# Optimization experiments

Hardware: AMD Instinct MI355X
Metric: run time of the kernel (lower is better)

## Reference

```python
import jax, jax.numpy as jnp
import numpy as np

N_LAYERS = 2
D_MODEL = 1024
D_INNER = 2048  # expand=2
D_STATE = 16
D_CONV = 4
DT_RANK = 64    # ceil(d_model/16)
N_CLASSES = 10
B, L = 4, 1024


def setup_inputs() -> dict:
    key = jax.random.key(0)
    ks = jax.random.split(key, 20)
    s = 0.02
    inp = {
        'x': jax.random.normal(ks[0], (B, L, D_MODEL), jnp.float32),
        'ln1_w': jnp.ones((N_LAYERS, D_MODEL), jnp.float32),
        'ln1_b': jnp.zeros((N_LAYERS, D_MODEL), jnp.float32),
        'in_proj_w': jax.random.normal(ks[1], (N_LAYERS, 2 * D_INNER, D_MODEL), jnp.float32) * s,
        'conv_w': jax.random.normal(ks[2], (N_LAYERS, D_INNER, D_CONV), jnp.float32) * 0.2,
        'conv_b': jnp.zeros((N_LAYERS, D_INNER), jnp.float32),
        'x_proj_w': jax.random.normal(ks[3], (N_LAYERS, DT_RANK + 2 * D_STATE, D_INNER), jnp.float32) * s,
        'dt_proj_w': jax.random.normal(ks[4], (N_LAYERS, D_INNER, DT_RANK), jnp.float32) * 0.1,
        'dt_proj_b': jax.random.normal(ks[5], (N_LAYERS, D_INNER), jnp.float32) * 0.1 - 4.6,  # softplus -> dt ~ 0.01
        'A_log': jnp.broadcast_to(jnp.log(jnp.arange(1, D_STATE + 1, dtype=jnp.float32)), (N_LAYERS, D_INNER, D_STATE)) + 0.0,
        'D_param': jnp.ones((N_LAYERS, D_INNER), jnp.float32),
        'out_proj_w': jax.random.normal(ks[6], (N_LAYERS, D_MODEL, D_INNER), jnp.float32) * s,
        'norm_w': jnp.ones((D_MODEL,), jnp.float32),
        'norm_b': jnp.zeros((D_MODEL,), jnp.float32),
        'head_w': jax.random.normal(ks[7], (N_CLASSES, D_MODEL), jnp.float32) * s,
        'head_b': jnp.zeros((N_CLASSES,), jnp.float32),
    }
    return inp


def _layernorm(x, w, b, eps=1e-5):
    mu = jnp.mean(x, axis=-1, keepdims=True)
    var = jnp.var(x, axis=-1, keepdims=True)
    return (x - mu) * jax.lax.rsqrt(var + eps) * w + b


def _selective_scan(xc, dt, A, Bm, Cm, D):
    # xc, dt: (B, L, D_INNER); Bm, Cm: (B, L, D_STATE); A: (D_INNER, D_STATE); D: (D_INNER,)
    def step(h, inp):
        dt_t, B_t, C_t, xc_t = inp  # (B,C),(B,N),(B,N),(B,C)
        dA = jnp.exp(dt_t[..., None] * A)            # (B, C, N)
        h = dA * h + (dt_t * xc_t)[..., None] * B_t[:, None, :]
        y = jnp.einsum('bcn,bn->bc', h, C_t)
        return h, y

    h0 = jnp.zeros((xc.shape[0], A.shape[0], A.shape[1]), xc.dtype)
    xs = (dt.transpose(1, 0, 2), Bm.transpose(1, 0, 2), Cm.transpose(1, 0, 2), xc.transpose(1, 0, 2))
    _, ys = jax.lax.scan(step, h0, xs)
    y = ys.transpose(1, 0, 2)  # (B, L, C)
    return y + xc * D


def _mamba_layer(x, ln_w, ln_b, in_w, cw, cb, xp_w, dtp_w, dtp_b, A_log, D, out_w):
    h = _layernorm(x, ln_w, ln_b)
    xz = jnp.einsum('bld,ed->ble', h, in_w)          # (B, L, 2*D_INNER)
    x_in, z = jnp.split(xz, 2, axis=-1)
    # causal depthwise conv1d, kernel D_CONV
    xp = jnp.pad(x_in, ((0, 0), (D_CONV - 1, 0), (0, 0)))
    conv = cb
    for k in range(D_CONV):
        conv = conv + cw[:, k] * xp[:, k:k + x_in.shape[1], :]
    xc = jax.nn.silu(conv)
    x_dbl = jnp.einsum('blc,ec->ble', xc, xp_w)
    dt_r = x_dbl[..., :DT_RANK]
    Bm = x_dbl[..., DT_RANK:DT_RANK + D_STATE]
    Cm = x_dbl[..., DT_RANK + D_STATE:]
    dt = jax.nn.softplus(jnp.einsum('blr,cr->blc', dt_r, dtp_w) + dtp_b)
    A = -jnp.exp(A_log)
    y = _selective_scan(xc, dt, A, Bm, Cm, D)
    y = y * jax.nn.silu(z)
    return x + jnp.einsum('blc,dc->bld', y, out_w)


def reference(x, ln1_w, ln1_b, in_proj_w, conv_w, conv_b, x_proj_w, dt_proj_w, dt_proj_b,
              A_log, D_param, out_proj_w, norm_w, norm_b, head_w, head_b):
    for i in range(N_LAYERS):
        x = _mamba_layer(x, ln1_w[i], ln1_b[i], in_proj_w[i], conv_w[i], conv_b[i],
                         x_proj_w[i], dt_proj_w[i], dt_proj_b[i], A_log[i], D_param[i], out_proj_w[i])
    x = _layernorm(x, norm_w, norm_b)
    pooled = jnp.mean(x, axis=1)  # (B, D_MODEL)
    return pooled @ head_w.T + head_b
```

## Files before the change

kernel.cpp:

```cpp
#include <hip/hip_runtime.h>
#include <hip/hip_bf16.h>

#define N_LAYERS 2
#define D_MODEL 1024
#define D_INNER 2048
#define D_STATE 16
#define D_CONV 4
#define DT_RANK 64
#define N_CLASSES 10
#define BB 4
#define LL 1024
#define BL (BB*LL)
#define CH 32
#define CLEN (LL/CH)
#define KS 8
#define KSO 2

typedef __attribute__((ext_vector_type(8))) short bf16x8;
typedef __attribute__((ext_vector_type(8))) unsigned short us8;
typedef __attribute__((ext_vector_type(4))) float f32x4;

typedef const void __attribute__((address_space(1)))* gas_ptr;
typedef void __attribute__((address_space(3)))* las_ptr;
#define GLDS16(g, p) __builtin_amdgcn_global_load_lds((gas_ptr)(g), (las_ptr)(p), 16, 0, 0)

__device__ inline unsigned short rnd_bf16(float x) {
  unsigned u = __float_as_uint(x);
  return (unsigned short)((u + 0x7FFFu + ((u >> 16) & 1u)) >> 16);
}
__device__ inline float b2f(unsigned short u) {
  return __uint_as_float(((unsigned)u) << 16);
}

__global__ __launch_bounds__(256) void round_k(const float* __restrict__ in,
    unsigned short* __restrict__ hi) {
  const int i = blockIdx.x * 256 + threadIdx.x;
  const float4 v = ((const float4*)in)[i];
  ushort4 h4;
  h4.x = rnd_bf16(v.x); h4.y = rnd_bf16(v.y);
  h4.z = rnd_bf16(v.z); h4.w = rnd_bf16(v.w);
  ((ushort4*)hi)[i] = h4;
}

__global__ __launch_bounds__(256) void layernorm_bf16_k(const float* __restrict__ x,
    const float* __restrict__ w, const float* __restrict__ b,
    unsigned short* __restrict__ oh) {
  const int row = blockIdx.x;
  const int t = threadIdx.x;
  const float4 v = *(const float4*)(x + (size_t)row * D_MODEL + t * 4);
  float s = v.x + v.y + v.z + v.w;
  float q = v.x*v.x + v.y*v.y + v.z*v.z + v.w*v.w;
  #pragma unroll
  for (int o = 32; o; o >>= 1) { s += __shfl_down(s, o); q += __shfl_down(q, o); }
  __shared__ float red[8];
  if ((t & 63) == 0) { red[t >> 6] = s; red[4 + (t >> 6)] = q; }
  __syncthreads();
  s = red[0] + red[1] + red[2] + red[3];
  q = red[4] + red[5] + red[6] + red[7];
  const float mean = s * (1.f / D_MODEL);
  const float var  = q * (1.f / D_MODEL) - mean * mean;
  const float rstd = rsqrtf(var + 1e-5f);
  const float4 wv = *(const float4*)(w + t * 4);
  const float4 bv = *(const float4*)(b + t * 4);
  ushort4 h4;
  h4.x = rnd_bf16((v.x - mean) * rstd * wv.x + bv.x);
  h4.y = rnd_bf16((v.y - mean) * rstd * wv.y + bv.y);
  h4.z = rnd_bf16((v.z - mean) * rstd * wv.z + bv.z);
  h4.w = rnd_bf16((v.w - mean) * rstd * wv.w + bv.w);
  ((ushort4*)(oh + (size_t)row * D_MODEL))[t] = h4;
}

template<int OUT>
__global__ __launch_bounds__(256) void oreduce_ln_k(
    const float* __restrict__ part, const float* __restrict__ Xin,
    float* __restrict__ Xout,
    const float* __restrict__ w, const float* __restrict__ b,
    void* __restrict__ out) {
  const int row = blockIdx.x;
  const int t = threadIdx.x;
  float4 v = *(const float4*)(Xin + (size_t)row * D_MODEL + t * 4);
  #pragma unroll
  for (int k = 0; k < KSO; k++) {
    const float4 p = *(const float4*)(part + (size_t)k * BL * D_MODEL
                                      + (size_t)row * D_MODEL + t * 4);
    v.x += p.x; v.y += p.y; v.z += p.z; v.w += p.w;
  }
  *(float4*)(Xout + (size_t)row * D_MODEL + t * 4) = v;
  float s = v.x + v.y + v.z + v.w;
  float q = v.x*v.x + v.y*v.y + v.z*v.z + v.w*v.w;
  #pragma unroll
  for (int o = 32; o; o >>= 1) { s += __shfl_down(s, o); q += __shfl_down(q, o); }
  __shared__ float red[8];
  if ((t & 63) == 0) { red[t >> 6] = s; red[4 + (t >> 6)] = q; }
  __syncthreads();
  s = red[0] + red[1] + red[2] + red[3];
  q = red[4] + red[5] + red[6] + red[7];
  const float mean = s * (1.f / D_MODEL);
  const float var  = q * (1.f / D_MODEL) - mean * mean;
  const float rstd = rsqrtf(var + 1e-5f);
  const float4 wv = *(const float4*)(w + t * 4);
  const float4 bv = *(const float4*)(b + t * 4);
  float4 o4;
  o4.x = (v.x - mean) * rstd * wv.x + bv.x;
  o4.y = (v.y - mean) * rstd * wv.y + bv.y;
  o4.z = (v.z - mean) * rstd * wv.z + bv.z;
  o4.w = (v.w - mean) * rstd * wv.w + bv.w;
  if constexpr (OUT == 0) {
    ushort4 h4;
    h4.x = rnd_bf16(o4.x); h4.y = rnd_bf16(o4.y);
    h4.z = rnd_bf16(o4.z); h4.w = rnd_bf16(o4.w);
    ((ushort4*)((unsigned short*)out + (size_t)row * D_MODEL))[t] = h4;
  } else {
    *(float4*)((float*)out + (size_t)row * D_MODEL + t * 4) = o4;
  }
}

template<int EPI, int KSEG>
__global__ __launch_bounds__(256) void mfma_gemm_nt(
    const unsigned short* __restrict__ Ah, const unsigned short* __restrict__ Bh,
    void* __restrict__ Cv, int M, int N, int K, int ldc) {
  __shared__ unsigned short As[128 * 64];
  __shared__ unsigned short Bs[128 * 64];
  const int tid = threadIdx.x;
  const int w = tid >> 6, l = tid & 63;
  const int wr = w >> 1, wc = w & 1;
  const int nbx = gridDim.x;
  const int nwg = nbx * gridDim.y;
  int bid = blockIdx.y * nbx + blockIdx.x;
  bid = (bid & 7) * (nwg >> 3) + (bid >> 3);
  const int st = bid >> 6, wi = bid & 63;
  const int stpr = nbx >> 3;
  const int n0 = ((st % stpr) * 8 + (wi & 7)) * 128;
  const int m0 = ((st / stpr) * 8 + (wi >> 3)) * 128;
  const int kz = (KSEG > 1) ? blockIdx.z : 0;
  const int kbeg = kz * (K / KSEG);
  const int kend = kbeg + K / KSEG;
  const int srow = l >> 3;
  const int scol = (l & 7) * 8;
  const int fr = l & 15;
  const int fk = (l >> 4) * 8;
  f32x4 acc[4][4] = {};

  #pragma unroll 1
  for (int k0 = kbeg; k0 < kend; k0 += 64) {
    __syncthreads();
    #pragma unroll
    for (int it = 0; it < 4; ++it) {
      const int bi = it * 4 + w;
      const int row = bi * 8 + srow;
      GLDS16(Ah + (size_t)(m0 + row) * K + k0 + scol, &As[bi * 512 + l * 8]);
      GLDS16(Bh + (size_t)(n0 + row) * K + k0 + scol, &Bs[bi * 512 + l * 8]);
    }
    __syncthreads();
    #pragma unroll
    for (int kk = 0; kk < 64; kk += 32) {
      bf16x8 a[4], b[4];
      #pragma unroll
      for (int f = 0; f < 4; ++f)
        b[f] = *(const bf16x8*)&Bs[(wc * 64 + f * 16 + fr) * 64 + kk + fk];
      #pragma unroll
      for (int f = 0; f < 4; ++f)
        a[f] = *(const bf16x8*)&As[(wr * 64 + f * 16 + fr) * 64 + kk + fk];
      #pragma unroll
      for (int i = 0; i < 4; ++i)
        #pragma unroll
        for (int j = 0; j < 4; ++j)
          acc[i][j] = __builtin_amdgcn_mfma_f32_16x16x32_bf16(
              a[i], b[j], acc[i][j], 0, 0, 0);
    }
  }
  const int orow = (l >> 4) * 4;
  const int ocol = l & 15;
  if constexpr (EPI == 0) {
    unsigned short* Cw = (unsigned short*)Cv;
    #pragma unroll
    for (int i = 0; i < 4; ++i)
      #pragma unroll
      for (int j = 0; j < 4; ++j)
        #pragma unroll
        for (int r = 0; r < 4; ++r) {
          const int m = m0 + wr * 64 + i * 16 + orow + r;
          const int n = n0 + wc * 64 + j * 16 + ocol;
          Cw[(size_t)m * ldc + n] = rnd_bf16(acc[i][j][r]);
        }
  } else {
    float* Cw = (float*)Cv + (size_t)kz * M * ldc;
    #pragma unroll
    for (int i = 0; i < 4; ++i)
      #pragma unroll
      for (int j = 0; j < 4; ++j)
        #pragma unroll
        for (int r = 0; r < 4; ++r) {
          const int m = m0 + wr * 64 + i * 16 + orow + r;
          const int n = n0 + wc * 64 + j * 16 + ocol;
          Cw[(size_t)m * ldc + n] = acc[i][j][r];
        }
  }
}

template<int BM, int BN, int BK, int TM, int TN, int EPI>
__global__ __launch_bounds__(256) void sgemm_nt(
    const float* __restrict__ A, const float* __restrict__ B,
    void* __restrict__ Cv, int M, int N, int K, int lda, int ldb, int ldc,
    const float* __restrict__ bias) {
  constexpr int THREADS = 256;
  constexpr int NT = BN / TN;
  constexpr int K4 = BK / 4;
  constexpr int A_F4 = BM * BK / (THREADS * 4);
  constexpr int B_F4 = BN * BK / (THREADS * 4);
  static_assert((BM / TM) * (BN / TN) == THREADS, "thread shape");
  __shared__ float As[BK][BM + 4];
  __shared__ float Bs[BK][BN + 4];
  const int tid = threadIdx.x;
  const int m0 = blockIdx.y * BM;
  const int n0 = blockIdx.x * BN;
  const int tn = (tid % NT) * TN;
  const int tm = (tid / NT) * TM;
  float acc[TM][TN] = {};
  for (int k0 = 0; k0 < K; k0 += BK) {
    #pragma unroll
    for (int i = 0; i < A_F4; i++) {
      int li = tid + i * THREADS;
      int r = li / K4, c4 = li % K4;
      float4 v = *(const float4*)(A + (size_t)(m0 + r) * lda + k0 + c4 * 4);
      As[c4*4+0][r] = v.x; As[c4*4+1][r] = v.y; As[c4*4+2][r] = v.z; As[c4*4+3][r] = v.w;
    }
    #pragma unroll
    for (int i = 0; i < B_F4; i++) {
      int li = tid + i * THREADS;
      int r = li / K4, c4 = li % K4;
      float4 v = *(const float4*)(B + (size_t)(n0 + r) * ldb + k0 + c4 * 4);
      Bs[c4*4+0][r] = v.x; Bs[c4*4+1][r] = v.y; Bs[c4*4+2][r] = v.z; Bs[c4*4+3][r] = v.w;
    }
    __syncthreads();
    #pragma unroll
    for (int k = 0; k < BK; k++) {
      float a[TM], bf[TN];
      #pragma unroll
      for (int i = 0; i < TM; i++) a[i] = As[k][tm + i];
      #pragma unroll
      for (int j = 0; j < TN; j++) bf[j] = Bs[k][tn + j];
      #pragma unroll
      for (int i = 0; i < TM; i++)
        #pragma unroll
        for (int j = 0; j < TN; j++)
          acc[i][j] = fmaf(a[i], bf[j], acc[i][j]);
    }
    __syncthreads();
  }
  #pragma unroll
  for (int i = 0; i < TM; i++) {
    const int m = m0 + tm + i;
    #pragma unroll
    for (int j = 0; j < TN; j++) {
      const int n = n0 + tn + j;
      float v = acc[i][j];
      if constexpr (EPI == 1) {
        v += bias[n];
        v = (v > 20.f) ? v : log1pf(__expf(v));
        ((unsigned short*)Cv)[(size_t)m * ldc + n] = rnd_bf16(v);
      } else {
        ((float*)Cv)[(size_t)m * ldc + n] = v;
      }
    }
  }
}

__global__ __launch_bounds__(256) void sgemm_splitk_k(
    const unsigned short* __restrict__ A, const float* __restrict__ B,
    float* __restrict__ part) {
  __shared__ float As[32][64 + 4];
  __shared__ float Bs[32][32 + 4];
  const int tid = threadIdx.x;
  const int n0 = blockIdx.x * 32;
  const int m0 = blockIdx.y * 64;
  const int kz = blockIdx.z;
  const int tn = (tid & 15) * 2;
  const int tm = (tid >> 4) * 4;
  float acc[4][2] = {};
  for (int kb = 0; kb < 256; kb += 32) {
    const int k0 = kz * 256 + kb;
    {
      int r = tid >> 2, c8 = (tid & 3) * 8;
      us8 u = *(const us8*)(A + (size_t)(m0 + r) * D_INNER + k0 + c8);
      #pragma unroll
      for (int j = 0; j < 8; j++) As[c8 + j][r] = b2f((unsigned short)u[j]);
    }
    {
      int r = tid >> 3, c4 = tid & 7;
      float4 v = *(const float4*)(B + (size_t)(n0 + r) * D_INNER + k0 + c4 * 4);
      Bs[c4*4+0][r] = v.x; Bs[c4*4+1][r] = v.y;
      Bs[c4*4+2][r] = v.z; Bs[c4*4+3][r] = v.w;
    }
    __syncthreads();
    #pragma unroll
    for (int k = 0; k < 32; k++) {
      float a[4], bf[2];
      #pragma unroll
      for (int i = 0; i < 4; i++) a[i] = As[k][tm + i];
      bf[0] = Bs[k][tn]; bf[1] = Bs[k][tn + 1];
      #pragma unroll
      for (int i = 0; i < 4; i++) {
        acc[i][0] = fmaf(a[i], bf[0], acc[i][0]);
        acc[i][1] = fmaf(a[i], bf[1], acc[i][1]);
      }
    }
    __syncthreads();
  }
  float* p = part + (size_t)kz * BL * 96;
  #pragma unroll
  for (int i = 0; i < 4; i++) {
    const int m = m0 + tm + i;
    p[(size_t)m * 96 + n0 + tn]     = acc[i][0];
    p[(size_t)m * 96 + n0 + tn + 1] = acc[i][1];
  }
}

__global__ __launch_bounds__(256) void xproj_reduce_k(
    const float* __restrict__ part, float* __restrict__ out) {
  const int i = blockIdx.x * 256 + threadIdx.x;
  float s = 0.f;
  #pragma unroll
  for (int k = 0; k < KS; k++) s += part[(size_t)k * BL * 96 + i];
  out[i] = s;
}

__global__ __launch_bounds__(256) void conv_silu_k(
    const unsigned short* __restrict__ xz,
    const float* __restrict__ cw, const float* __restrict__ cb,
    unsigned short* __restrict__ xc) {
  const int gid = blockIdx.x * 256 + threadIdx.x;
  const int c4 = (gid & (D_INNER / 4 - 1)) << 2;
  const int row = gid >> 9;
  const int l = row & (LL - 1);
  const unsigned short* base = xz + (size_t)row * (2 * D_INNER) + c4;
  const float4 w0 = *(const float4*)(cw + (c4 + 0) * 4);
  const float4 w1 = *(const float4*)(cw + (c4 + 1) * 4);
  const float4 w2 = *(const float4*)(cw + (c4 + 2) * 4);
  const float4 w3 = *(const float4*)(cw + (c4 + 3) * 4);
  float4 acc = *(const float4*)(cb + c4);
  ushort4 uv = *(const ushort4*)base;
  acc.x = fmaf(w0.w, b2f(uv.x), acc.x); acc.y = fmaf(w1.w, b2f(uv.y), acc.y);
  acc.z = fmaf(w2.w, b2f(uv.z), acc.z); acc.w = fmaf(w3.w, b2f(uv.w), acc.w);
  if (l >= 1) {
    uv = *(const ushort4*)(base - 2 * D_INNER);
    acc.x = fmaf(w0.z, b2f(uv.x), acc.x); acc.y = fmaf(w1.z, b2f(uv.y), acc.y);
    acc.z = fmaf(w2.z, b2f(uv.z), acc.z); acc.w = fmaf(w3.z, b2f(uv.w), acc.w);
  }
  if (l >= 2) {
    uv = *(const ushort4*)(base - 4 * D_INNER);
    acc.x = fmaf(w0.y, b2f(uv.x), acc.x); acc.y = fmaf(w1.y, b2f(uv.y), acc.y);
    acc.z = fmaf(w2.y, b2f(uv.z), acc.z); acc.w = fmaf(w3.y, b2f(uv.w), acc.w);
  }
  if (l >= 3) {
    uv = *(const ushort4*)(base - 6 * D_INNER);
    acc.x = fmaf(w0.x, b2f(uv.x), acc.x); acc.y = fmaf(w1.x, b2f(uv.y), acc.y);
    acc.z = fmaf(w2.x, b2f(uv.z), acc.z); acc.w = fmaf(w3.x, b2f(uv.w), acc.w);
  }
  ushort4 o4;
  o4.x = rnd_bf16(acc.x / (1.f + __expf(-acc.x)));
  o4.y = rnd_bf16(acc.y / (1.f + __expf(-acc.y)));
  o4.z = rnd_bf16(acc.z / (1.f + __expf(-acc.z)));
  o4.w = rnd_bf16(acc.w / (1.f + __expf(-acc.w)));
  *(ushort4*)(xc + (size_t)row * D_INNER + c4) = o4;
}

__global__ __launch_bounds__(256) void scan_pass1_k(
    const unsigned short* __restrict__ dt, const unsigned short* __restrict__ xc,
    const float* __restrict__ xdbl, const float* __restrict__ A_log,
    float* __restrict__ hend, float* __restrict__ sumdt) {
  const int c = blockIdx.x * 256 + threadIdx.x;
  const int k = blockIdx.y;
  const int b = blockIdx.z;
  float Ac[D_STATE];
  #pragma unroll
  for (int n = 0; n < D_STATE; n++) Ac[n] = -__expf(A_log[c * D_STATE + n]);
  float h[D_STATE] = {};
  float sd = 0.f;
  const size_t r0 = (size_t)b * LL + (size_t)k * CLEN;
  const unsigned short* dtp = dt + r0 * D_INNER + c;
  const unsigned short* xcp = xc + r0 * D_INNER + c;
  const float* Bp  = xdbl + r0 * 96 + DT_RANK;

  float dtv = b2f(dtp[0]);
  float xv  = b2f(xcp[0]);
  float4 B0 = *(const float4*)(Bp + 0);
  float4 B1 = *(const float4*)(Bp + 4);
  float4 B2 = *(const float4*)(Bp + 8);
  float4 B3 = *(const float4*)(Bp + 12);
  for (int l = 0; l < CLEN; l++) {
    const int lp = (l + 1 < CLEN) ? l + 1 : l;
    const float dtv2 = b2f(dtp[(size_t)lp * D_INNER]);
    const float xv2  = b2f(xcp[(size_t)lp * D_INNER]);
    const float4 B0n = *(const float4*)(Bp + (size_t)lp * 96 + 0);
    const float4 B1n = *(const float4*)(Bp + (size_t)lp * 96 + 4);
    const float4 B2n = *(const float4*)(Bp + (size_t)lp * 96 + 8);
    const float4 B3n = *(const float4*)(Bp + (size_t)lp * 96 + 12);
    sd += dtv;
    const float dx = dtv * xv;
    const float Bv[D_STATE] = {B0.x,B0.y,B0.z,B0.w, B1.x,B1.y,B1.z,B1.w,
                               B2.x,B2.y,B2.z,B2.w, B3.x,B3.y,B3.z,B3.w};
    #pragma unroll
    for (int n = 0; n < D_STATE; n++)
      h[n] = fmaf(__expf(dtv * Ac[n]), h[n], dx * Bv[n]);
    dtv = dtv2; xv = xv2; B0 = B0n; B1 = B1n; B2 = B2n; B3 = B3n;
  }
  float* he = hend + (((size_t)(b * CH + k) * D_INNER + c) << 4);
  #pragma unroll
  for (int n = 0; n < D_STATE; n += 4)
    *(float4*)(he + n) = make_float4(h[n], h[n+1], h[n+2], h[n+3]);
  sumdt[(size_t)(b * CH + k) * D_INNER + c] = sd;
}

__global__ __launch_bounds__(256) void scan_fix_k(
    float* __restrict__ hend, const float* __restrict__ sumdt,
    const float* __restrict__ A_log) {
  const int gid = blockIdx.x * 256 + threadIdx.x;
  const int n = gid & 15;
  const int c = (gid >> 4) & (D_INNER - 1);
  const int b = gid >> 15;
  const float Ac = -__expf(A_log[c * D_STATE + n]);
  float hrun = 0.f;
  for (int k = 0; k < CH; k++) {
    const size_t base = (size_t)(b * CH + k) * D_INNER + c;
    const float sd = sumdt[base];
    float* hp = hend + (base << 4) + n;
    const float tmp = *hp;
    *hp = hrun;
    hrun = fmaf(__expf(Ac * sd), hrun, tmp);
  }
}

__global__ __launch_bounds__(256) void scan_pass3_k(
    const unsigned short* __restrict__ dt, const unsigned short* __restrict__ xc,
    const float* __restrict__ xdbl, const unsigned short* __restrict__ xz,
    const float* __restrict__ h0, const float* __restrict__ A_log,
    const float* __restrict__ Dp, unsigned short* __restrict__ yh) {
  const int c = blockIdx.x * 256 + threadIdx.x;
  const int k = blockIdx.y;
  const int b = blockIdx.z;
  float Ac[D_STATE];
  #pragma unroll
  for (int n = 0; n < D_STATE; n++) Ac[n] = -__expf(A_log[c * D_STATE + n]);
  const float Dv = Dp[c];
  float h[D_STATE];
  const float* hp = h0 + (((size_t)(b * CH + k) * D_INNER + c) << 4);
  #pragma unroll
  for (int n = 0; n < D_STATE; n += 4) {
    const float4 v = *(const float4*)(hp + n);
    h[n] = v.x; h[n+1] = v.y; h[n+2] = v.z; h[n+3] = v.w;
  }
  const size_t r0 = (size_t)b * LL + (size_t)k * CLEN;
  const unsigned short* dtp = dt + r0 * D_INNER + c;
  const unsigned short* xcp = xc + r0 * D_INNER + c;
  const float* Bp  = xdbl + r0 * 96 + DT_RANK;
  const unsigned short* zp = xz + r0 * (size_t)(2 * D_INNER) + D_INNER + c;
  unsigned short* yhp = yh + r0 * D_INNER + c;

  float dtv = b2f(dtp[0]);
  float xv  = b2f(xcp[0]);
  float zv  = b2f(zp[0]);
  float4 B0 = *(const float4*)(Bp + 0);
  float4 B1 = *(const float4*)(Bp + 4);
  float4 B2 = *(const float4*)(Bp + 8);
  float4 B3 = *(const float4*)(Bp + 12);
  float4 C0 = *(const float4*)(Bp + 16);
  float4 C1 = *(const float4*)(Bp + 20);
  float4 C2 = *(const float4*)(Bp + 24);
  float4 C3 = *(const float4*)(Bp + 28);
  for (int l = 0; l < CLEN; l++) {
    const int lp = (l + 1 < CLEN) ? l + 1 : l;
    const float dtv2 = b2f(dtp[(size_t)lp * D_INNER]);
    const float xv2  = b2f(xcp[(size_t)lp * D_INNER]);
    const float zv2  = b2f(zp[(size_t)lp * 2 * D_INNER]);
    const float4 B0n = *(const float4*)(Bp + (size_t)lp * 96 + 0);
    const float4 B1n = *(const float4*)(Bp + (size_t)lp * 96 + 4);
    const float4 B2n = *(const float4*)(Bp + (size_t)lp * 96 + 8);
    const float4 B3n = *(const float4*)(Bp + (size_t)lp * 96 + 12);
    const float4 C0n = *(const float4*)(Bp + (size_t)lp * 96 + 16);
    const float4 C1n = *(const float4*)(Bp + (size_t)lp * 96 + 20);
    const float4 C2n = *(const float4*)(Bp + (size_t)lp * 96 + 24);
    const float4 C3n = *(const float4*)(Bp + (size_t)lp * 96 + 28);
    const float dx = dtv * xv;
    const float Bv[D_STATE] = {B0.x,B0.y,B0.z,B0.w, B1.x,B1.y,B1.z,B1.w,
                               B2.x,B2.y,B2.z,B2.w, B3.x,B3.y,B3.z,B3.w};
    const float Cv[D_STATE] = {C0.x,C0.y,C0.z,C0.w, C1.x,C1.y,C1.z,C1.w,
                               C2.x,C2.y,C2.z,C2.w, C3.x,C3.y,C3.z,C3.w};
    float y = 0.f;
    #pragma unroll
    for (int n = 0; n < D_STATE; n++) {
      h[n] = fmaf(__expf(dtv * Ac[n]), h[n], dx * Bv[n]);
      y = fmaf(h[n], Cv[n], y);
    }
    y = fmaf(xv, Dv, y);
    y *= zv / (1.f + __expf(-zv));
    yhp[(size_t)l * D_INNER] = rnd_bf16(y);
    dtv = dtv2; xv = xv2; zv = zv2;
    B0 = B0n; B1 = B1n; B2 = B2n; B3 = B3n;
    C0 = C0n; C1 = C1n; C2 = C2n; C3 = C3n;
  }
}

__global__ __launch_bounds__(256) void pool1_k(const float* __restrict__ h,
    float* __restrict__ pp) {
  const int d = blockIdx.x * 256 + threadIdx.x;
  const int b = blockIdx.y;
  const int seg = blockIdx.z;
  float s = 0.f;
  const size_t base = (size_t)b * LL + (size_t)seg * 64;
  for (int l = 0; l < 64; l++) s += h[(base + l) * D_MODEL + d];
  pp[((size_t)(b * 16 + seg)) * D_MODEL + d] = s;
}
__global__ __launch_bounds__(256) void pool2_k(const float* __restrict__ pp,
    float* __restrict__ pooled) {
  const int d = blockIdx.x * 256 + threadIdx.x;
  const int b = blockIdx.y;
  float s = 0.f;
  #pragma unroll
  for (int k = 0; k < 16; k++) s += pp[((size_t)(b * 16 + k)) * D_MODEL + d];
  pooled[b * D_MODEL + d] = s * (1.f / LL);
}

__global__ __launch_bounds__(64) void head_k(const float* __restrict__ pooled,
    const float* __restrict__ hw, const float* __restrict__ hb,
    float* __restrict__ out) {
  const int b = blockIdx.x / N_CLASSES;
  const int j = blockIdx.x % N_CLASSES;
  float s = 0.f;
  for (int k = threadIdx.x; k < D_MODEL; k += 64)
    s = fmaf(pooled[b * D_MODEL + k], hw[j * D_MODEL + k], s);
  #pragma unroll
  for (int o = 32; o; o >>= 1) s += __shfl_down(s, o);
  if (threadIdx.x == 0) out[b * N_CLASSES + j] = s + hb[j];
}

extern "C" void kernel_launch(void* const* d_in, const int* in_sizes, int n_in,
                              void* d_out, int out_size, void* d_ws, size_t ws_size,
                              hipStream_t stream) {
  const float* x0    = (const float*)d_in[0];
  const float* ln1w  = (const float*)d_in[1];
  const float* ln1b  = (const float*)d_in[2];
  const float* inw   = (const float*)d_in[3];
  const float* convw = (const float*)d_in[4];
  const float* convb = (const float*)d_in[5];
  const float* xpw   = (const float*)d_in[6];
  const float* dtpw  = (const float*)d_in[7];
  const float* dtpb  = (const float*)d_in[8];
  const float* Alog  = (const float*)d_in[9];
  const float* Dp    = (const float*)d_in[10];
  const float* outw  = (const float*)d_in[11];
  const float* normw = (const float*)d_in[12];
  const float* normb = (const float*)d_in[13];
  const float* headw = (const float*)d_in[14];
  const float* headb = (const float*)d_in[15];

  float* ws = (float*)d_ws;
  size_t f = 0;
  float* X      = ws + f; f += (size_t)BL * D_MODEL;
  float* xzf    = ws + f; f += (size_t)BL * D_INNER;
  float* xdbl   = ws + f; f += (size_t)BL * 96;
  float* dty    = ws + f; f += (size_t)BL * D_INNER;
  float* pooled = ws + f; f += 4096;
  float* pooldp = ws + f; f += (size_t)16 * BB * D_MODEL;
  float* xpart  = ws + f; f += (size_t)KS * BL * 96;
  float* hend   = ws + f; f += (size_t)BB * CH * D_INNER * D_STATE;
  float* opart  = ws + f; f += (size_t)KSO * BL * D_MODEL;
  unsigned short* hh  = (unsigned short*)(ws + f); f += (size_t)BL * D_MODEL / 2;
  unsigned short* yh  = (unsigned short*)(ws + f); f += (size_t)BL * D_INNER / 2;
  unsigned short* xcb = (unsigned short*)(ws + f); f += (size_t)BL * D_INNER / 2;
  unsigned short* wih = (unsigned short*)(ws + f);
  f += (size_t)N_LAYERS * 2 * D_INNER * D_MODEL / 2;
  unsigned short* woh = (unsigned short*)(ws + f);
  f += (size_t)N_LAYERS * D_MODEL * D_INNER / 2;
  unsigned short* xz  = (unsigned short*)xzf;
  unsigned short* dtb = (unsigned short*)dty;
  float* sumdt = xpart;

  round_k<<<(N_LAYERS * 2 * D_INNER * D_MODEL) / 1024, 256, 0, stream>>>(inw, wih);
  round_k<<<(N_LAYERS * D_MODEL * D_INNER) / 1024, 256, 0, stream>>>(outw, woh);
  layernorm_bf16_k<<<BL, 256, 0, stream>>>(x0, ln1w, ln1b, hh);

  for (int layer = 0; layer < N_LAYERS; ++layer) {
    const unsigned short* wi = wih + (size_t)layer * 2 * D_INNER * D_MODEL;
    const unsigned short* wo = woh + (size_t)layer * D_MODEL * D_INNER;
    mfma_gemm_nt<0, 1><<<dim3(4096 / 128, 4096 / 128), 256, 0, stream>>>(
        hh, wi, xz, BL, 2 * D_INNER, D_MODEL, 2 * D_INNER);
    conv_silu_k<<<(BL * D_INNER / 4) / 256, 256, 0, stream>>>(
        xz, convw + layer * D_INNER * D_CONV, convb + layer * D_INNER, xcb);
    sgemm_splitk_k<<<dim3(96 / 32, 4096 / 64, KS), 256, 0, stream>>>(
        xcb, xpw + (size_t)layer * 96 * D_INNER, xpart);
    xproj_reduce_k<<<(BL * 96) / 256, 256, 0, stream>>>(xpart, xdbl);
    sgemm_nt<64,64,64,4,4,1><<<dim3(2048 / 64, 4096 / 64), 256, 0, stream>>>(
        xdbl, dtpw + (size_t)layer * D_INNER * DT_RANK, dtb,
        BL, D_INNER, DT_RANK, 96, DT_RANK, D_INNER,
        dtpb + layer * D_INNER);
    scan_pass1_k<<<dim3(D_INNER / 256, CH, BB), 256, 0, stream>>>(
        dtb, xcb, xdbl, Alog + (size_t)layer * D_INNER * D_STATE, hend, sumdt);
    scan_fix_k<<<(BB * D_INNER * D_STATE) / 256, 256, 0, stream>>>(
        hend, sumdt, Alog + (size_t)layer * D_INNER * D_STATE);
    scan_pass3_k<<<dim3(D_INNER / 256, CH, BB), 256, 0, stream>>>(
        dtb, xcb, xdbl, xz, hend, Alog + (size_t)layer * D_INNER * D_STATE,
        Dp + layer * D_INNER, yh);
    mfma_gemm_nt<1, KSO><<<dim3(1024 / 128, 4096 / 128, KSO), 256, 0, stream>>>(
        yh, wo, opart, BL, D_MODEL, D_INNER, D_MODEL);
    const float* Xin = (layer == 0) ? x0 : X;
    if (layer + 1 < N_LAYERS) {
      oreduce_ln_k<0><<<BL, 256, 0, stream>>>(
          opart, Xin, X, ln1w + (layer + 1) * D_MODEL,
          ln1b + (layer + 1) * D_MODEL, hh);
    } else {
      oreduce_ln_k<1><<<BL, 256, 0, stream>>>(opart, Xin, X, normw, normb, dty);
    }
  }

  pool1_k<<<dim3(D_MODEL / 256, BB, 16), 256, 0, stream>>>(dty, pooldp);
  pool2_k<<<dim3(D_MODEL / 256, BB), 256, 0, stream>>>(pooldp, pooled);
  head_k<<<BB * N_CLASSES, 64, 0, stream>>>(pooled, headw, headb, (float*)d_out);
}
```

Baseline: 603.2 us.

## Add 256x256-tile double-buffered MFMA GEMM for the input projection

Adds a new bf16 MFMA GEMM kernel for the in_proj GEMM (4096x4096x1024). It uses 256x256 output tiles, 512 threads, an XOR-swizzled LDS layout, a two-stage global_load_lds prefetch pipeline and s_setprio around the MFMA bursts. The larger tile gives more data reuse per LDS load and overlaps loads with compute. In exchange it needs 128KB of LDS, so only one block fits per CU, and it writes the output with scalar bf16 stores. The old 128-tile kernel also gains a fallback block mapping for grids narrower than 8 tiles.

```diff
diff --git a/kernel.cpp b/kernel.cpp
--- a/kernel.cpp
+++ b/kernel.cpp
@@ -115,6 +115,94 @@
   }
 }
 
+__global__ __launch_bounds__(512) void mfma_gemm256_nt(
+    const unsigned short* __restrict__ A, const unsigned short* __restrict__ B,
+    unsigned short* __restrict__ C, int K, int ldc) {
+  __shared__ unsigned short S[65536];
+  const int tid = threadIdx.x;
+  const int l = tid & 63;
+  const int w = tid >> 6;
+  const int wm = w >> 2, wn = w & 3;
+  const int bid = blockIdx.y * 16 + blockIdx.x;
+  const int x = bid & 7, v = bid >> 3;
+  const int bx = (x & 1) * 8 + (v & 7);
+  const int by = (x >> 1) * 4 + (v >> 3);
+  const int m0 = by * 256, n0 = bx * 256;
+  const int nkt = K >> 6;
+  const int r8 = (tid >> 3) & 7;
+  const int c16s = (tid & 7) ^ r8;
+
+  auto stage1 = [&](int kt, int mat, int half) {
+    const unsigned short* base = (mat == 0) ? (A + (size_t)m0 * K)
+                                            : (B + (size_t)n0 * K);
+    unsigned short* dst = S + ((kt & 1) * 32768 + mat * 16384 + half * 8192);
+    #pragma unroll
+    for (int e = 0; e < 2; ++e) {
+      const int row = half * 128 + e * 64 + (tid >> 3);
+      GLDS16(base + (size_t)row * K + kt * 64 + c16s * 8,
+             dst + e * 4096 + tid * 8);
+    }
+  };
+  auto stage_full = [&](int kt) {
+    stage1(kt, 0, 0); stage1(kt, 0, 1); stage1(kt, 1, 0); stage1(kt, 1, 1);
+  };
+
+  stage_full(0);
+  if (nkt > 1) stage_full(1);
+
+  f32x4 acc[8][4] = {};
+  const int fr = l & 15;
+  const int fk8 = l >> 4;
+
+  #pragma unroll 1
+  for (int kt = 0; kt < nkt; ++kt) {
+    if (kt + 1 < nkt) asm volatile("s_waitcnt vmcnt(8)" ::: "memory");
+    else              asm volatile("s_waitcnt vmcnt(0)" ::: "memory");
+    __builtin_amdgcn_s_barrier();
+    __builtin_amdgcn_sched_barrier(0);
+    const unsigned short* SA = S + (kt & 1) * 32768;
+    const unsigned short* SB = SA + 16384;
+    #pragma unroll
+    for (int kk8 = 0; kk8 < 8; kk8 += 4) {
+      bf16x8 av[8], bv[4];
+      const int c8 = kk8 + fk8;
+      #pragma unroll
+      for (int i = 0; i < 8; ++i) {
+        const int R = wm * 128 + i * 16 + fr;
+        av[i] = *(const bf16x8*)&SA[R * 64 + ((c8 ^ (R & 7)) << 3)];
+      }
+      #pragma unroll
+      for (int j = 0; j < 4; ++j) {
+        const int R = wn * 64 + j * 16 + fr;
+        bv[j] = *(const bf16x8*)&SB[R * 64 + ((c8 ^ (R & 7)) << 3)];
+      }
+      __builtin_amdgcn_s_setprio(1);
+      #pragma unroll
+      for (int i = 0; i < 8; ++i)
+        #pragma unroll
+        for (int j = 0; j < 4; ++j)
+          acc[i][j] = __builtin_amdgcn_mfma_f32_16x16x32_bf16(
+              av[i], bv[j], acc[i][j], 0, 0, 0);
+      __builtin_amdgcn_s_setprio(0);
+    }
+    __builtin_amdgcn_s_barrier();
+    __builtin_amdgcn_sched_barrier(0);
+    if (kt + 2 < nkt) stage_full(kt + 2);
+  }
+
+  const int orow = (l >> 4) * 4, ocol = l & 15;
+  #pragma unroll
+  for (int i = 0; i < 8; ++i)
+    #pragma unroll
+    for (int j = 0; j < 4; ++j)
+      #pragma unroll
+      for (int r = 0; r < 4; ++r) {
+        const int m = m0 + wm * 128 + i * 16 + orow + r;
+        const int n = n0 + wn * 64 + j * 16 + ocol;
+        C[(size_t)m * ldc + n] = rnd_bf16(acc[i][j][r]);
+      }
+}
+
 template<int EPI, int KSEG>
 __global__ __launch_bounds__(256) void mfma_gemm_nt(
     const unsigned short* __restrict__ Ah, const unsigned short* __restrict__ Bh,
@@ -129,9 +217,15 @@
   int bid = blockIdx.y * nbx + blockIdx.x;
   bid = (bid & 7) * (nwg >> 3) + (bid >> 3);
   const int st = bid >> 6, wi = bid & 63;
-  const int stpr = nbx >> 3;
-  const int n0 = ((st % stpr) * 8 + (wi & 7)) * 128;
-  const int m0 = ((st / stpr) * 8 + (wi >> 3)) * 128;
+  const int stpr = (nbx >= 8) ? (nbx >> 3) : 1;
+  int n0, m0;
+  if (nbx >= 8) {
+    n0 = ((st % stpr) * 8 + (wi & 7)) * 128;
+    m0 = ((st / stpr) * 8 + (wi >> 3)) * 128;
+  } else {
+    n0 = (bid % nbx) * 128;
+    m0 = (bid / nbx) * 128;
+  }
   const int kz = (KSEG > 1) ? blockIdx.z : 0;
   const int kbeg = kz * (K / KSEG);
   const int kend = kbeg + K / KSEG;
@@ -583,8 +677,8 @@
   for (int layer = 0; layer < N_LAYERS; ++layer) {
     const unsigned short* wi = wih + (size_t)layer * 2 * D_INNER * D_MODEL;
     const unsigned short* wo = woh + (size_t)layer * D_MODEL * D_INNER;
-    mfma_gemm_nt<0, 1><<<dim3(4096 / 128, 4096 / 128), 256, 0, stream>>>(
-        hh, wi, xz, BL, 2 * D_INNER, D_MODEL, 2 * D_INNER);
+    mfma_gemm256_nt<<<dim3(16, 16), 512, 0, stream>>>(
+        hh, wi, xz, D_MODEL, 2 * D_INNER);
     conv_silu_k<<<(BL * D_INNER / 4) / 256, 256, 0, stream>>>(
         xz, convw + layer * D_INNER * D_CONV, convb + layer * D_INNER, xcb);
     sgemm_splitk_k<<<dim3(96 / 32, 4096 / 64, KS), 256, 0, stream>>>(
```

After: 570.7 us. 1.06x faster.
